# Performance work log

Measured on AMD Instinct MI355X. Metric: run time of the kernel, lower is better.

## Reference

```python
import jax, jax.numpy as jnp
import numpy as np

H = 16   # num_attention_heads
G = 4    # num_gqa_groups
D = 64   # head_dim = hidden // H
HIDDEN = 1024
KV_DIM = HIDDEN // H * G  # 256
EPS = 1e-5


def setup_inputs() -> dict:
    key = jax.random.key(0)
    k0, k1, k2, k3 = jax.random.split(key, 4)
    x = jax.random.normal(k0, (8, 4096, HIDDEN), dtype=jnp.float32)
    query_weight = jax.random.normal(k1, (HIDDEN, HIDDEN), dtype=jnp.float32) * 0.02
    key_weight = jax.random.normal(k2, (KV_DIM, HIDDEN), dtype=jnp.float32) * 0.02
    value_weight = jax.random.normal(k3, (KV_DIM, HIDDEN), dtype=jnp.float32) * 0.02
    return {
        "x": x,
        "query_weight": query_weight,
        "key_weight": key_weight,
        "value_weight": value_weight,
        "query_bias": jnp.zeros((HIDDEN,), jnp.float32),
        "key_bias": jnp.zeros((KV_DIM,), jnp.float32),
        "value_bias": jnp.zeros((KV_DIM,), jnp.float32),
        "layer_norm_weight": jnp.ones((HIDDEN,), jnp.float32),
        "layer_norm_bias": jnp.zeros((HIDDEN,), jnp.float32),
    }


def reference(x, query_weight, key_weight, value_weight, query_bias, key_bias,
              value_bias, layer_norm_weight, layer_norm_bias):
    b, s, _ = x.shape
    # Shared LayerNorm (q is k is v path in apply_qkv_norm)
    mu = jnp.mean(x, axis=-1, keepdims=True)
    var = jnp.mean(jnp.square(x - mu), axis=-1, keepdims=True)
    xn = (x - mu) * jax.lax.rsqrt(var + EPS) * layer_norm_weight + layer_norm_bias
    # Q/K/V projections (F.linear: x @ W.T + b)
    q = xn @ query_weight.T + query_bias           # [b, s, H*D]
    k = xn @ key_weight.T + key_bias               # [b, s, G*1*D]
    v = xn @ value_weight.T + value_bias           # [b, s, G*1*D]
    # 'b s (h d) -> b h s d'
    q = q.reshape(b, s, H, D).transpose(0, 2, 1, 3)           # [b, H, s, D]
    # 'b s (g h d) -> b h (g s) d' with h = KV_DIM//(G*D) = 1
    def kv_rearrange(t):
        t = t.reshape(b, s, G, 1, D)                          # b s g h d
        t = t.transpose(0, 3, 2, 1, 4)                        # b h g s d
        return t.reshape(b, 1, G * s, D)                      # [b, 1, G*s, D]
    return q, kv_rearrange(k), kv_rearrange(v)
```

## Files before the change

kernel.cpp:

```cpp
#include <hip/hip_runtime.h>
#include <hip/hip_bf16.h>


#define HIDDEN 1024
#define NTOK   32768

typedef __bf16 bf16x8 __attribute__((ext_vector_type(8)));
typedef float  f32x4  __attribute__((ext_vector_type(4)));

#define GLOBAL_AS(p) ((const __attribute__((address_space(1))) void*)(p))
#define LDS_AS(p)    ((__attribute__((address_space(3))) void*)(p))

__device__ __forceinline__ unsigned short f2bf(float f) {
  union { float f; unsigned int i; } x; x.f = f;
  unsigned int r = x.i + 0x7FFFu + ((x.i >> 16) & 1u);
  return (unsigned short)(r >> 16);
}

__global__ __launch_bounds__(256) void ln_cvt_kernel(
    const float* __restrict__ x,
    const float* __restrict__ gamma,
    const float* __restrict__ beta,
    const float* __restrict__ wq,
    const float* __restrict__ wk,
    const float* __restrict__ wv,
    unsigned short* __restrict__ xn,
    unsigned short* __restrict__ wb) {
  const int bid = blockIdx.x;
  const int t   = threadIdx.x;
  if (bid < NTOK) {
    const size_t base = (size_t)bid * HIDDEN;
    const float4 v = ((const float4*)(x + base))[t];
    float s  = v.x + v.y + v.z + v.w;
    float s2 = v.x*v.x + v.y*v.y + v.z*v.z + v.w*v.w;
#pragma unroll
    for (int off = 32; off >= 1; off >>= 1) {
      s  += __shfl_xor(s,  off);
      s2 += __shfl_xor(s2, off);
    }
    __shared__ float red[8];
    const int w = t >> 6;
    if ((t & 63) == 0) { red[w] = s; red[4 + w] = s2; }
    __syncthreads();
    s  = red[0] + red[1] + red[2] + red[3];
    s2 = red[4] + red[5] + red[6] + red[7];
    const float mu   = s * (1.0f / HIDDEN);
    const float rstd = rsqrtf(s2 * (1.0f / HIDDEN) - mu * mu + 1e-5f);
    const float4 g  = ((const float4*)gamma)[t];
    const float4 bb = ((const float4*)beta)[t];
    ushort4 o;
    o.x = f2bf((v.x - mu) * rstd * g.x + bb.x);
    o.y = f2bf((v.y - mu) * rstd * g.y + bb.y);
    o.z = f2bf((v.z - mu) * rstd * g.z + bb.z);
    o.w = f2bf((v.w - mu) * rstd * g.w + bb.w);
    ((ushort4*)(xn + base))[t] = o;
  } else {
    const int b2 = bid - NTOK;
    const float* src;
    int off;
    if (b2 < 1024)      { src = wq; off = b2; }
    else if (b2 < 1280) { src = wk; off = b2 - 1024; }
    else                { src = wv; off = b2 - 1280; }
    const float4 v = ((const float4*)src)[off * 256 + t];
    ushort4 o;
    o.x = f2bf(v.x); o.y = f2bf(v.y); o.z = f2bf(v.z); o.w = f2bf(v.w);
    ((ushort4*)wb)[b2 * 256 + t] = o;
  }
}

__global__ __launch_bounds__(256, 4) void qkv_gemm(
    const unsigned short* __restrict__ xn,
    const unsigned short* __restrict__ wqb,
    const float* __restrict__ bq,
    const float* __restrict__ bk,
    const float* __restrict__ bv,
    float* __restrict__ out) {
  __shared__ unsigned short lds[16384];
  unsigned short* Alds = lds;
  unsigned short* Blds = lds + 8192;

  const int bid = blockIdx.x;
  const int swz = (bid & 7) * 384 + (bid >> 3);
  const int mt  = swz / 12;
  const int nt  = swz % 12;
  const int brow = mt * 128;

  const unsigned short* wbase; const float* biasptr;
  int segcol; size_t obase; int hg;
  if (nt < 8)        { wbase = wqb + (size_t)nt * 128 * HIDDEN;            biasptr = bq; segcol = nt * 128;        obase = 0u;        hg = 16; }
  else if (nt < 10)  { wbase = wqb + (size_t)(1024 + (nt - 8) * 128) * HIDDEN;  biasptr = bk; segcol = (nt - 8) * 128;  obase = 33554432u; hg = 4; }
  else               { wbase = wqb + (size_t)(1280 + (nt - 10) * 128) * HIDDEN; biasptr = bv; segcol = (nt - 10) * 128; obase = 41943040u; hg = 4; }

  const int t = threadIdx.x;
  const int w = t >> 6, lane = t & 63;
  const int wm = w >> 1, wn = w & 1;
  const int l15 = lane & 15, hi = lane >> 4;

  const int sr  = w * 32 + (lane >> 2);
  const int scg = ((lane & 3) ^ ((lane >> 3) & 3)) * 8;
  const unsigned short* aST = xn    + (size_t)(brow + sr) * HIDDEN + scg;
  const unsigned short* bST = wbase + (size_t)sr * HIDDEN + scg;
  const int ldsq = w * 1024;

  const int rdx  = (hi ^ ((l15 >> 1) & 3)) * 8;
  const int rowA = wm * 64 + l15;
  const int rowB = wn * 64 + l15;

  f32x4 acc[4][4];
#pragma unroll
  for (int m = 0; m < 4; ++m)
#pragma unroll
    for (int n = 0; n < 4; ++n) acc[m][n] = (f32x4){0.f, 0.f, 0.f, 0.f};
  bf16x8 a[4], b[4];

#define STA(BUF, KT) do {                                                       \
    unsigned short* _d = Alds + (BUF) * 4096 + ldsq;                            \
    const unsigned short* _s = aST + (size_t)((KT) * 32);                       \
    __builtin_amdgcn_global_load_lds(GLOBAL_AS(_s), LDS_AS(_d), 16, 0, 0);      \
    __builtin_amdgcn_global_load_lds(GLOBAL_AS(_s + 16 * HIDDEN), LDS_AS(_d + 512), 16, 0, 0); \
  } while (0)
#define STB(BUF, KT) do {                                                       \
    unsigned short* _d = Blds + (BUF) * 4096 + ldsq;                            \
    const unsigned short* _s = bST + (size_t)((KT) * 32);                       \
    __builtin_amdgcn_global_load_lds(GLOBAL_AS(_s), LDS_AS(_d), 16, 0, 0);      \
    __builtin_amdgcn_global_load_lds(GLOBAL_AS(_s + 16 * HIDDEN), LDS_AS(_d + 512), 16, 0, 0); \
  } while (0)
#define RD(BUF) do { _Pragma("unroll")                                          \
    for (int m = 0; m < 4; ++m)                                                 \
      a[m] = *(const bf16x8*)(Alds + (BUF) * 4096 + (rowA + m * 16) * 32 + rdx);\
    _Pragma("unroll")                                                           \
    for (int n = 0; n < 4; ++n)                                                 \
      b[n] = *(const bf16x8*)(Blds + (BUF) * 4096 + (rowB + n * 16) * 32 + rdx);\
  } while (0)
#define MMX do { _Pragma("unroll")                                              \
    for (int m = 0; m < 4; ++m)                                                 \
      _Pragma("unroll") for (int n = 0; n < 4; ++n)                             \
        acc[m][n] = __builtin_amdgcn_mfma_f32_16x16x32_bf16(a[m], b[n], acc[m][n], 0, 0, 0); \
  } while (0)
#define PIN __builtin_amdgcn_sched_barrier(0)

  STA(0, 0); STB(0, 0);
  asm volatile("s_waitcnt vmcnt(0)" ::: "memory");
  PIN;
  __builtin_amdgcn_s_barrier();
  PIN;

#pragma unroll 2
  for (int T = 0; T < 31; ++T) {
    const int buf = T & 1;
    RD(buf);
    STA(buf ^ 1, T + 1);
    STB(buf ^ 1, T + 1);
    PIN;
    asm volatile("s_waitcnt lgkmcnt(0)" ::: "memory");
    PIN;
    MMX;
    asm volatile("s_waitcnt vmcnt(0)" ::: "memory");
    PIN;
    __builtin_amdgcn_s_barrier();
    PIN;
  }
  RD(1);
  asm volatile("s_waitcnt lgkmcnt(0)" ::: "memory");
  PIN;
  MMX;
  __builtin_amdgcn_s_barrier();
  PIN;

#undef STA
#undef STB
#undef RD
#undef MMX
#undef PIN

  float* ep = (float*)lds;
  const int epb = w * 1344;
  const int headcol = segcol + wn * 64;
  const int gidx = headcol >> 6;
  const int tok0 = brow + wm * 64;
  const int b_ = tok0 >> 12;
  float* wout = out + obase + (size_t)(b_ * hg + gidx) * 262144u
                    + (size_t)(tok0 & 4095) * 64u;
  float biasv[4];
#pragma unroll
  for (int n = 0; n < 4; ++n) biasv[n] = biasptr[headcol + n * 16 + l15];

#pragma unroll
  for (int m = 0; m < 4; ++m) {
#pragma unroll
    for (int n = 0; n < 4; ++n)
#pragma unroll
      for (int j = 0; j < 4; ++j)
        ep[epb + (hi * 4 + j) * 84 + n * 16 + l15] = acc[m][n][j] + biasv[n];
    asm volatile("s_waitcnt lgkmcnt(0)" ::: "memory");
#pragma unroll
    for (int it = 0; it < 4; ++it) {
      const int r = it * 4 + hi;
      const float4 v = *(const float4*)(ep + epb + r * 84 + l15 * 4);
      *(float4*)(wout + (size_t)(m * 16 + r) * 64 + l15 * 4) = v;
    }
  }
}

extern "C" void kernel_launch(void* const* d_in, const int* in_sizes, int n_in,
                              void* d_out, int out_size, void* d_ws, size_t ws_size,
                              hipStream_t stream) {
  const float* x  = (const float*)d_in[0];
  const float* wq = (const float*)d_in[1];
  const float* wk = (const float*)d_in[2];
  const float* wv = (const float*)d_in[3];
  const float* bq = (const float*)d_in[4];
  const float* bk = (const float*)d_in[5];
  const float* bv = (const float*)d_in[6];
  const float* g  = (const float*)d_in[7];
  const float* be = (const float*)d_in[8];
  float* out = (float*)d_out;

  unsigned short* xn = (unsigned short*)d_ws;
  unsigned short* wb = (unsigned short*)((char*)d_ws + (64u << 20));

  ln_cvt_kernel<<<NTOK + 1536, 256, 0, stream>>>(x, g, be, wq, wk, wv, xn, wb);
  qkv_gemm<<<3072, 256, 0, stream>>>(xn, wb, bq, bk, bv, out);
}
```

Baseline: 186.0 us.

## Triple-buffer GEMM LDS tiles with two-stage-ahead prefetch

```diff
diff --git a/kernel.cpp b/kernel.cpp
--- a/kernel.cpp
+++ b/kernel.cpp
@@ -68,16 +68,16 @@
   }
 }
 
-__global__ __launch_bounds__(256, 4) void qkv_gemm(
+__global__ __launch_bounds__(256, 3) void qkv_gemm(
     const unsigned short* __restrict__ xn,
     const unsigned short* __restrict__ wqb,
     const float* __restrict__ bq,
     const float* __restrict__ bk,
     const float* __restrict__ bv,
     float* __restrict__ out) {
-  __shared__ unsigned short lds[16384];
+  __shared__ unsigned short lds[24576];
   unsigned short* Alds = lds;
-  unsigned short* Blds = lds + 8192;
+  unsigned short* Blds = lds + 12288;
 
   const int bid = blockIdx.x;
   const int swz = (bid & 7) * 384 + (bid >> 3);
@@ -87,7 +87,7 @@
 
   const unsigned short* wbase; const float* biasptr;
   int segcol; size_t obase; int hg;
-  if (nt < 8)        { wbase = wqb + (size_t)nt * 128 * HIDDEN;            biasptr = bq; segcol = nt * 128;        obase = 0u;        hg = 16; }
+  if (nt < 8)        { wbase = wqb + (size_t)nt * 128 * HIDDEN;                 biasptr = bq; segcol = nt * 128;        obase = 0u;        hg = 16; }
   else if (nt < 10)  { wbase = wqb + (size_t)(1024 + (nt - 8) * 128) * HIDDEN;  biasptr = bk; segcol = (nt - 8) * 128;  obase = 33554432u; hg = 4; }
   else               { wbase = wqb + (size_t)(1280 + (nt - 10) * 128) * HIDDEN; biasptr = bv; segcol = (nt - 10) * 128; obase = 41943040u; hg = 4; }
 
@@ -113,17 +113,15 @@
     for (int n = 0; n < 4; ++n) acc[m][n] = (f32x4){0.f, 0.f, 0.f, 0.f};
   bf16x8 a[4], b[4];
 
-#define STA(BUF, KT) do {                                                       \
-    unsigned short* _d = Alds + (BUF) * 4096 + ldsq;                            \
-    const unsigned short* _s = aST + (size_t)((KT) * 32);                       \
-    __builtin_amdgcn_global_load_lds(GLOBAL_AS(_s), LDS_AS(_d), 16, 0, 0);      \
-    __builtin_amdgcn_global_load_lds(GLOBAL_AS(_s + 16 * HIDDEN), LDS_AS(_d + 512), 16, 0, 0); \
-  } while (0)
-#define STB(BUF, KT) do {                                                       \
-    unsigned short* _d = Blds + (BUF) * 4096 + ldsq;                            \
-    const unsigned short* _s = bST + (size_t)((KT) * 32);                       \
-    __builtin_amdgcn_global_load_lds(GLOBAL_AS(_s), LDS_AS(_d), 16, 0, 0);      \
-    __builtin_amdgcn_global_load_lds(GLOBAL_AS(_s + 16 * HIDDEN), LDS_AS(_d + 512), 16, 0, 0); \
+#define ST(BUF, KT) do {                                                        \
+    unsigned short* _da = Alds + (BUF) * 4096 + ldsq;                           \
+    unsigned short* _db = Blds + (BUF) * 4096 + ldsq;                           \
+    const unsigned short* _sa = aST + (size_t)((KT) * 32);                      \
+    const unsigned short* _sb = bST + (size_t)((KT) * 32);                      \
+    __builtin_amdgcn_global_load_lds(GLOBAL_AS(_sa), LDS_AS(_da), 16, 0, 0);    \
+    __builtin_amdgcn_global_load_lds(GLOBAL_AS(_sa + 16 * HIDDEN), LDS_AS(_da + 512), 16, 0, 0); \
+    __builtin_amdgcn_global_load_lds(GLOBAL_AS(_sb), LDS_AS(_db), 16, 0, 0);    \
+    __builtin_amdgcn_global_load_lds(GLOBAL_AS(_sb + 16 * HIDDEN), LDS_AS(_db + 512), 16, 0, 0); \
   } while (0)
 #define RD(BUF) do { _Pragma("unroll")                                          \
     for (int m = 0; m < 4; ++m)                                                 \
@@ -138,40 +136,34 @@
         acc[m][n] = __builtin_amdgcn_mfma_f32_16x16x32_bf16(a[m], b[n], acc[m][n], 0, 0, 0); \
   } while (0)
 #define PIN __builtin_amdgcn_sched_barrier(0)
-
-  STA(0, 0); STB(0, 0);
-  asm volatile("s_waitcnt vmcnt(0)" ::: "memory");
-  PIN;
-  __builtin_amdgcn_s_barrier();
-  PIN;
-
-#pragma unroll 2
-  for (int T = 0; T < 31; ++T) {
-    const int buf = T & 1;
-    RD(buf);
-    STA(buf ^ 1, T + 1);
-    STB(buf ^ 1, T + 1);
-    PIN;
-    asm volatile("s_waitcnt lgkmcnt(0)" ::: "memory");
-    PIN;
-    MMX;
-    asm volatile("s_waitcnt vmcnt(0)" ::: "memory");
-    PIN;
-    __builtin_amdgcn_s_barrier();
-    PIN;
+#define LGKM0 asm volatile("s_waitcnt lgkmcnt(0)" ::: "memory")
+#define VMW(N) asm volatile("s_waitcnt vmcnt(" #N ")" ::: "memory")
+#define BAR __builtin_amdgcn_s_barrier()
+
+#define STEP(BUF, SBUF, T) do {                                                 \
+    ST(SBUF, (T) + 2); RD(BUF); PIN; LGKM0; PIN; MMX;                           \
+    VMW(4); PIN; BAR; PIN;                                                      \
+  } while (0)
+
+  ST(0, 0); ST(1, 1);
+  VMW(4); PIN; BAR; PIN;
+
+  for (int T = 0; T < 30; T += 3) {
+    STEP(0, 2, T);
+    STEP(1, 0, T + 1);
+    STEP(2, 1, T + 2);
   }
-  RD(1);
-  asm volatile("s_waitcnt lgkmcnt(0)" ::: "memory");
-  PIN;
-  MMX;
-  __builtin_amdgcn_s_barrier();
-  PIN;
-
-#undef STA
-#undef STB
+  RD(0); PIN; LGKM0; PIN; MMX; VMW(0); PIN; BAR; PIN;
+  RD(1); PIN; LGKM0; PIN; MMX;
+  BAR;
+
+#undef ST
 #undef RD
 #undef MMX
-#undef PIN
+#undef STEP
+#undef LGKM0
+#undef VMW
+#undef BAR
 
   float* ep = (float*)lds;
   const int epb = w * 1344;
@@ -200,6 +192,7 @@
       *(float4*)(wout + (size_t)(m * 16 + r) * 64 + l15 * 4) = v;
     }
   }
+#undef PIN
 }
 
 extern "C" void kernel_launch(void* const* d_in, const int* in_sizes, int n_in,
```

Measured after the change: 181.4 us. 1.03x faster.
